# Kernel tuning notes

Measured on AMD Instinct MI355X. Metric: run time of the kernel, lower is better.

Reference implementation:

```python
import jax, jax.numpy as jnp
import numpy as np

B, S, DIM, H = 4, 2048, 1024, 16
DEPTH = DIM // H


def setup_inputs() -> dict:
    key = jax.random.key(0)
    ks = jax.random.split(key, 12)
    s = 0.02
    return {
        "Q": jax.random.normal(ks[0], (B, S, DIM), jnp.float32),
        "K": jax.random.normal(ks[1], (B, S, DIM), jnp.float32),
        "V": jax.random.normal(ks[2], (B, S, DIM), jnp.float32),
        "mask": jax.random.randint(ks[3], (B, 1, 1, S), 0, 2).astype(jnp.float32),
        "Wq": jax.random.normal(ks[4], (DIM, DIM), jnp.float32) * s,
        "bq": jnp.zeros((DIM,), jnp.float32),
        "Wk": jax.random.normal(ks[5], (DIM, DIM), jnp.float32) * s,
        "bk": jnp.zeros((DIM,), jnp.float32),
        "Wv": jax.random.normal(ks[6], (DIM, DIM), jnp.float32) * s,
        "bv": jnp.zeros((DIM,), jnp.float32),
        "Wo": jax.random.normal(ks[7], (DIM, DIM), jnp.float32) * s,
        "bo": jnp.zeros((DIM,), jnp.float32),
    }


def _split_heads(x):
    # [B,S,DIM] -> [B,H,S,DEPTH]
    return x.reshape(x.shape[0], x.shape[1], H, DEPTH).transpose(0, 2, 1, 3)


def reference(Q, K, V, mask, Wq, bq, Wk, bk, Wv, bv, Wo, bo):
    q = _split_heads(Q @ Wq + bq)
    k = _split_heads(K @ Wk + bk)
    v = _split_heads(V @ Wv + bv)
    # scaled dot-product attention; note original scales by sqrt(depth) = last dim of K after split
    logits = jnp.einsum("bhqd,bhkd->bhqk", q, k) / jnp.sqrt(jnp.float32(DEPTH))
    logits = logits + mask * -1e9
    attn = jax.nn.softmax(logits, axis=-1)
    ctx = jnp.einsum("bhqk,bhkd->bhqd", attn, v)
    ctx = ctx.transpose(0, 2, 1, 3).reshape(Q.shape[0], Q.shape[1], DIM)
    return ctx @ Wo + bo
```

## Files before the change

kernel.cpp:

```cpp
#include <hip/hip_runtime.h>

typedef short s16x8 __attribute__((ext_vector_type(8)));
typedef short s16x4 __attribute__((ext_vector_type(4)));
typedef float f32x4 __attribute__((ext_vector_type(4)));

#define MFMA32(a, b, c) __builtin_amdgcn_mfma_f32_16x16x32_bf16((a), (b), (c), 0, 0, 0)

__device__ __forceinline__ void stage16(const unsigned short* g, unsigned short* l) {
#if defined(__HIP_DEVICE_COMPILE__)
  __builtin_amdgcn_global_load_lds((const __attribute__((address_space(1))) unsigned int*)g,
                                   (__attribute__((address_space(3))) unsigned int*)l, 16, 0, 0);
#endif
}

__device__ __forceinline__ unsigned short f2b(float f) {
  unsigned int u = __builtin_bit_cast(unsigned int, f);
  unsigned int r = u + 0x7FFFu + ((u >> 16) & 1u);
  return (unsigned short)(r >> 16);
}
__device__ __forceinline__ unsigned int pk2(float a, float b) {
#if defined(__HIP_DEVICE_COMPILE__)
  unsigned int ua = __builtin_bit_cast(unsigned int, a);
  unsigned int ub = __builtin_bit_cast(unsigned int, b);
  ua += 0x7FFFu + ((ua >> 16) & 1u);
  ub += 0x7FFFu + ((ub >> 16) & 1u);
  return __builtin_amdgcn_perm(ub, ua, 0x07060302u);
#else
  return (unsigned int)f2b(a) | ((unsigned int)f2b(b) << 16);
#endif
}
__device__ __forceinline__ float fast_exp2(float x) {
#if defined(__HIP_DEVICE_COMPILE__) && __has_builtin(__builtin_amdgcn_exp2f)
  return __builtin_amdgcn_exp2f(x);
#else
  return exp2f(x);
#endif
}

__global__ __launch_bounds__(256) void castq(const float* __restrict__ X,
                                             unsigned short* __restrict__ Y) {
  int i = blockIdx.x * 256 + threadIdx.x;
  float4 f0 = ((const float4*)X)[i * 2];
  float4 f1 = ((const float4*)X)[i * 2 + 1];
  uint4 u;
  u.x = pk2(f0.x, f0.y);
  u.y = pk2(f0.z, f0.w);
  u.z = pk2(f1.x, f1.y);
  u.w = pk2(f1.z, f1.w);
  ((uint4*)Y)[i] = u;
}

__global__ void wtrans(const float* __restrict__ W0, const float* __restrict__ W1,
                       const float* __restrict__ W2, const float* __restrict__ W3,
                       unsigned short* __restrict__ T0, unsigned short* __restrict__ T1,
                       unsigned short* __restrict__ T2, unsigned short* __restrict__ T3) {
  const float* W;
  unsigned short* T;
  switch (blockIdx.z) {
    case 0: W = W0; T = T0; break;
    case 1: W = W1; T = T1; break;
    case 2: W = W2; T = T2; break;
    default: W = W3; T = T3; break;
  }
  __shared__ float tile[32][33];
  const int n0 = blockIdx.x << 5;
  const int k0 = blockIdx.y << 5;
  const int tx = threadIdx.x;
  const int ty = threadIdx.y;
#pragma unroll
  for (int j = 0; j < 4; ++j)
    tile[ty + 8 * j][tx] = W[(size_t)(k0 + ty + 8 * j) * 1024 + n0 + tx];
  __syncthreads();
#pragma unroll
  for (int j = 0; j < 4; ++j)
    T[(size_t)(n0 + ty + 8 * j) * 1024 + k0 + tx] = f2b(tile[tx][ty + 8 * j]);
}

template <int MODE>
__global__ __launch_bounds__(256, 3) void gemm_bt(const unsigned short* __restrict__ A,
                                                  const unsigned short* __restrict__ Bt,
                                                  const float* __restrict__ bias,
                                                  void* __restrict__ Cout, float oscale) {
  __shared__ __align__(16) unsigned short As[2 * 128 * 32];
  __shared__ __align__(16) unsigned short Bs[2 * 128 * 32];
  const int n0 = blockIdx.x * 128;
  const int m0 = blockIdx.y * 128;
  const int tid = threadIdx.x;
  const int w = tid >> 6;
  const int lane = tid & 63;
  const int lr = lane & 15;
  const int lg = lane >> 4;
  const int wm = (w >> 1) << 6;
  const int wn = (w & 1) << 6;

  const int srow = w * 16 + (lane >> 2);
  const int sseg = lane & 3;
  const unsigned short* Ag0 = A + (size_t)(m0 + srow) * 1024 + sseg * 8;
  const unsigned short* Ag1 = A + (size_t)(m0 + 64 + srow) * 1024 + sseg * 8;
  const unsigned short* Bg0 = Bt + (size_t)(n0 + srow) * 1024 + sseg * 8;
  const unsigned short* Bg1 = Bt + (size_t)(n0 + 64 + srow) * 1024 + sseg * 8;
  unsigned short* Al0 = &As[(w * 16) * 32];
  unsigned short* Al1 = &As[(64 + w * 16) * 32];
  unsigned short* Bl0 = &Bs[(w * 16) * 32];
  unsigned short* Bl1 = &Bs[(64 + w * 16) * 32];

  f32x4 acc[4][4];
#pragma unroll
  for (int i = 0; i < 4; ++i)
#pragma unroll
    for (int j = 0; j < 4; ++j) {
      f32x4 z = {0.f, 0.f, 0.f, 0.f};
      acc[i][j] = z;
    }

  stage16(Ag0, Al0);
  stage16(Ag1, Al1);
  stage16(Bg0, Bl0);
  stage16(Bg1, Bl1);
  asm volatile("s_waitcnt vmcnt(0)\n\ts_barrier" ::: "memory");

  int cur = 0;
  for (int k0 = 0; k0 < 1024; k0 += 32) {
    if (k0 + 32 < 1024) {
      const int nb = (cur ^ 1) * 4096;
      stage16(Ag0 + k0 + 32, Al0 + nb);
      stage16(Ag1 + k0 + 32, Al1 + nb);
      stage16(Bg0 + k0 + 32, Bl0 + nb);
      stage16(Bg1 + k0 + 32, Bl1 + nb);
    }
    const int cb = cur * 4096;
    s16x8 af[4], bfr[4];
#pragma unroll
    for (int mt = 0; mt < 4; ++mt)
      af[mt] = *(const s16x8*)&As[cb + (wm + mt * 16 + lr) * 32 + lg * 8];
#pragma unroll
    for (int nt = 0; nt < 4; ++nt)
      bfr[nt] = *(const s16x8*)&Bs[cb + (wn + nt * 16 + lr) * 32 + lg * 8];
#pragma unroll
    for (int mt = 0; mt < 4; ++mt)
#pragma unroll
      for (int nt = 0; nt < 4; ++nt)
        acc[mt][nt] = MFMA32(af[mt], bfr[nt], acc[mt][nt]);
    asm volatile("s_waitcnt vmcnt(0)\n\ts_barrier" ::: "memory");
    cur ^= 1;
  }

  float bcol[4];
#pragma unroll
  for (int nt = 0; nt < 4; ++nt) bcol[nt] = bias[n0 + wn + nt * 16 + lr];

#pragma unroll
  for (int mt = 0; mt < 4; ++mt)
#pragma unroll
    for (int nt = 0; nt < 4; ++nt)
#pragma unroll
      for (int r = 0; r < 4; ++r) {
        float v = (acc[mt][nt][r] + bcol[nt]) * oscale;
        int row = m0 + wm + mt * 16 + lg * 4 + r;
        int col = n0 + wn + nt * 16 + lr;
        if constexpr (MODE == 0) {
          int b = row >> 11, s = row & 2047, hh = col >> 6, d = col & 63;
          ((unsigned short*)Cout)[(((size_t)(b * 16 + hh) * 2048 + s) << 6) + d] = f2b(v);
        } else if constexpr (MODE == 1) {
          int b = row >> 11, s = row & 2047, hh = col >> 6, d = col & 63;
          ((unsigned short*)Cout)[(((size_t)(b * 16 + hh) * 64 + d) << 11) + s] = f2b(v);
        } else {
          ((float*)Cout)[(size_t)row * 1024 + col] = v;
        }
      }
}

__global__ __launch_bounds__(256, 4) void flash_attn(const unsigned short* __restrict__ qh,
                                                     const unsigned short* __restrict__ kh,
                                                     const unsigned short* __restrict__ vt,
                                                     const float* __restrict__ mask,
                                                     unsigned short* __restrict__ ctx) {
  const float c2 = 1.4426950408889634e9f;
  const int id = blockIdx.x;
  const int bh = id & 63;
  const int qtile = id >> 6;
  const int b = bh >> 4;
  const int h = bh & 15;
  const int q0 = qtile << 7;
  const int tid = threadIdx.x;
  const int w = tid >> 6;
  const int lane = tid & 63;
  const int lr = lane & 15;
  const int lg = lane >> 4;

  __shared__ __align__(16) unsigned short Ks[2 * 64 * 64];
  __shared__ __align__(16) unsigned short Vs[2 * 64 * 64];

  const unsigned short* qbase = qh + ((size_t)bh * 2048 + q0 + w * 32) * 64;
  const unsigned short* kbase = kh + (size_t)bh * 2048 * 64;
  const unsigned short* vbase = vt + (size_t)bh * 64 * 2048;
  const float* mbase = mask + b * 2048;

  const int rowc = lane >> 3;
  const int gseg = (lane & 7) ^ rowc;
  const unsigned short* kg0 = kbase + (size_t)(w * 16 + rowc) * 64 + gseg * 8;
  const unsigned short* kg1 = kbase + (size_t)(w * 16 + 8 + rowc) * 64 + gseg * 8;
  const unsigned short* vg0 = vbase + (size_t)(w * 16 + rowc) * 2048 + gseg * 8;
  const unsigned short* vg1 = vbase + (size_t)(w * 16 + 8 + rowc) * 2048 + gseg * 8;
  unsigned short* kl0 = &Ks[(w * 16 + 0) * 64];
  unsigned short* kl1 = &Ks[(w * 16 + 8) * 64];
  unsigned short* vl0 = &Vs[(w * 16 + 0) * 64];
  unsigned short* vl1 = &Vs[(w * 16 + 8) * 64];

  s16x8 qf[2][2];
#pragma unroll
  for (int qt = 0; qt < 2; ++qt)
#pragma unroll
    for (int kk = 0; kk < 2; ++kk)
      qf[qt][kk] = *(const s16x8*)(qbase + (qt * 16 + lr) * 64 + kk * 32 + lg * 8);

  const s16x8 ones8 = {(short)0x3F80, (short)0x3F80, (short)0x3F80, (short)0x3F80,
                       (short)0x3F80, (short)0x3F80, (short)0x3F80, (short)0x3F80};

  f32x4 o_acc[2][4];
  f32x4 l_acc[2];
#pragma unroll
  for (int qt = 0; qt < 2; ++qt) {
    f32x4 z = {0.f, 0.f, 0.f, 0.f};
    l_acc[qt] = z;
#pragma unroll
    for (int dt = 0; dt < 4; ++dt) o_acc[qt][dt] = z;
  }

  stage16(kg0, kl0);
  stage16(kg1, kl1);
  stage16(vg0, vl0);
  stage16(vg1, vl1);
  asm volatile("s_waitcnt vmcnt(0)\n\ts_barrier" ::: "memory");

  int cur = 0;
  for (int t0 = 0; t0 < 2048; t0 += 64) {
    if (t0 + 64 < 2048) {
      const int nb = (cur ^ 1) * 4096;
      stage16(kg0 + (size_t)(t0 + 64) * 64, kl0 + nb);
      stage16(kg1 + (size_t)(t0 + 64) * 64, kl1 + nb);
      stage16(vg0 + (t0 + 64), vl0 + nb);
      stage16(vg1 + (t0 + 64), vl1 + nb);
    }
    float4 mk[4];
#pragma unroll
    for (int kt = 0; kt < 4; ++kt) mk[kt] = *(const float4*)(mbase + t0 + kt * 16 + lg * 4);

    const int cb = cur * 4096;
    const int sw = lr & 7;
    unsigned int pw[4][2][2];
#pragma unroll
    for (int kt = 0; kt < 4; ++kt) {
      const int krow = kt * 16 + lr;
      s16x8 kf0 = *(const s16x8*)&Ks[cb + krow * 64 + ((lg ^ sw) * 8)];
      s16x8 kf1 = *(const s16x8*)&Ks[cb + krow * 64 + (((4 + lg) ^ sw) * 8)];
      float ml0 = mk[kt].x * c2, ml1 = mk[kt].y * c2;
      float ml2 = mk[kt].z * c2, ml3 = mk[kt].w * c2;
#pragma unroll
      for (int qt = 0; qt < 2; ++qt) {
        f32x4 s = {0.f, 0.f, 0.f, 0.f};
        s = MFMA32(kf0, qf[qt][0], s);
        s = MFMA32(kf1, qf[qt][1], s);
        pw[kt][qt][0] = pk2(fast_exp2(s[0] - ml0), fast_exp2(s[1] - ml1));
        pw[kt][qt][1] = pk2(fast_exp2(s[2] - ml2), fast_exp2(s[3] - ml3));
      }
    }

#pragma unroll
    for (int c = 0; c < 2; ++c) {
      s16x8 pb[2];
#pragma unroll
      for (int qt = 0; qt < 2; ++qt) {
        uint4 u;
        u.x = pw[2 * c][qt][0];
        u.y = pw[2 * c][qt][1];
        u.z = pw[2 * c + 1][qt][0];
        u.w = pw[2 * c + 1][qt][1];
        pb[qt] = __builtin_bit_cast(s16x8, u);
        l_acc[qt] = MFMA32(ones8, pb[qt], l_acc[qt]);
      }
      const int plo = ((c << 2) | (lg >> 1)) ^ sw;
      const int phi = ((c << 2) | 2 | (lg >> 1)) ^ sw;
      const int sub = (lg & 1) * 4;
#pragma unroll
      for (int dt = 0; dt < 4; ++dt) {
        const int d = dt * 16 + lr;
        s16x4 vlo = *(const s16x4*)&Vs[cb + d * 64 + plo * 8 + sub];
        s16x4 vhi = *(const s16x4*)&Vs[cb + d * 64 + phi * 8 + sub];
        s16x8 vf = __builtin_shufflevector(vlo, vhi, 0, 1, 2, 3, 4, 5, 6, 7);
#pragma unroll
        for (int qt = 0; qt < 2; ++qt) o_acc[qt][dt] = MFMA32(vf, pb[qt], o_acc[qt][dt]);
      }
    }

    asm volatile("s_waitcnt vmcnt(0)\n\ts_barrier" ::: "memory");
    cur ^= 1;
  }

#pragma unroll
  for (int qt = 0; qt < 2; ++qt) {
    float inv = 1.0f / l_acc[qt][0];
    int q = q0 + w * 32 + qt * 16 + lr;
    unsigned short* cp = ctx + ((size_t)(b * 2048 + q) * 16 + h) * 64 + lg * 4;
#pragma unroll
    for (int dt = 0; dt < 4; ++dt) {
      f32x4 o = o_acc[qt][dt];
      uint2 u;
      u.x = pk2(o[0] * inv, o[1] * inv);
      u.y = pk2(o[2] * inv, o[3] * inv);
      *(uint2*)(cp + dt * 16) = u;
    }
  }
}

extern "C" void kernel_launch(void* const* d_in, const int* in_sizes, int n_in,
                              void* d_out, int out_size, void* d_ws, size_t ws_size,
                              hipStream_t stream) {
  (void)in_sizes; (void)n_in; (void)out_size; (void)ws_size;
  const float* Q = (const float*)d_in[0];
  const float* K = (const float*)d_in[1];
  const float* V = (const float*)d_in[2];
  const float* mask = (const float*)d_in[3];
  const float* Wq = (const float*)d_in[4];
  const float* bq = (const float*)d_in[5];
  const float* Wk = (const float*)d_in[6];
  const float* bk = (const float*)d_in[7];
  const float* Wv = (const float*)d_in[8];
  const float* bv = (const float*)d_in[9];
  const float* Wo = (const float*)d_in[10];
  const float* bo = (const float*)d_in[11];

  char* ws = (char*)d_ws;
  unsigned short* wqt = (unsigned short*)(ws + (size_t)0);
  unsigned short* wkt = (unsigned short*)(ws + ((size_t)2 << 20));
  unsigned short* wvt = (unsigned short*)(ws + ((size_t)4 << 20));
  unsigned short* wot = (unsigned short*)(ws + ((size_t)6 << 20));
  unsigned short* qhb = (unsigned short*)(ws + ((size_t)8 << 20));
  unsigned short* khb = (unsigned short*)(ws + ((size_t)24 << 20));
  unsigned short* vtb = (unsigned short*)(ws + ((size_t)40 << 20));
  unsigned short* tmp = (unsigned short*)(ws + ((size_t)56 << 20));
  unsigned short* ctx = tmp;

  wtrans<<<dim3(32, 32, 4), dim3(32, 8), 0, stream>>>(Wq, Wk, Wv, Wo, wqt, wkt, wvt, wot);

  const float qscale = 0.18033688011112042f;
  dim3 gg(8, 64), bb(256);
  const int castBlocks = (8192 * 1024) / (256 * 8);

  castq<<<castBlocks, 256, 0, stream>>>(Q, tmp);
  gemm_bt<0><<<gg, bb, 0, stream>>>(tmp, wqt, bq, qhb, qscale);
  castq<<<castBlocks, 256, 0, stream>>>(K, tmp);
  gemm_bt<0><<<gg, bb, 0, stream>>>(tmp, wkt, bk, khb, 1.0f);
  castq<<<castBlocks, 256, 0, stream>>>(V, tmp);
  gemm_bt<1><<<gg, bb, 0, stream>>>(tmp, wvt, bv, vtb, 1.0f);

  flash_attn<<<dim3(1024), dim3(256), 0, stream>>>(qhb, khb, vtb, mask, ctx);

  gemm_bt<2><<<gg, bb, 0, stream>>>(ctx, wot, bo, d_out, 1.0f);
}
```

Measured before the change: 389.3 us.

## Fuse fp32-to-bf16 cast into QKV GEMM and batch three projections in one launch

Removes the three separate castq kernels and their bf16 scratch round-trips. The new QKV GEMM loads fp32 activations directly, packs them to bf16 in registers and writes them to LDS, while B is still staged asynchronously. The three projections run as one grid with z=3 instead of three sequential launches. In exchange, each A tile reads twice the global bytes, and the conversion work sits inside the GEMM main loop, which may add latency.

```diff
diff --git a/kernel.cpp b/kernel.cpp
--- a/kernel.cpp
+++ b/kernel.cpp
@@ -35,19 +35,6 @@
 #else
   return exp2f(x);
 #endif
-}
-
-__global__ __launch_bounds__(256) void castq(const float* __restrict__ X,
-                                             unsigned short* __restrict__ Y) {
-  int i = blockIdx.x * 256 + threadIdx.x;
-  float4 f0 = ((const float4*)X)[i * 2];
-  float4 f1 = ((const float4*)X)[i * 2 + 1];
-  uint4 u;
-  u.x = pk2(f0.x, f0.y);
-  u.y = pk2(f0.z, f0.w);
-  u.z = pk2(f1.x, f1.y);
-  u.w = pk2(f1.z, f1.w);
-  ((uint4*)Y)[i] = u;
 }
 
 __global__ void wtrans(const float* __restrict__ W0, const float* __restrict__ W1,
@@ -76,11 +63,24 @@
     T[(size_t)(n0 + ty + 8 * j) * 1024 + k0 + tx] = f2b(tile[tx][ty + 8 * j]);
 }
 
-template <int MODE>
-__global__ __launch_bounds__(256, 3) void gemm_bt(const unsigned short* __restrict__ A,
-                                                  const unsigned short* __restrict__ Bt,
-                                                  const float* __restrict__ bias,
-                                                  void* __restrict__ Cout, float oscale) {
+__global__ __launch_bounds__(256, 3) void gemm_qkv(
+    const float* __restrict__ Qf, const float* __restrict__ Kf, const float* __restrict__ Vf,
+    const unsigned short* __restrict__ Wqt, const unsigned short* __restrict__ Wkt,
+    const unsigned short* __restrict__ Wvt, const float* __restrict__ bq,
+    const float* __restrict__ bk, const float* __restrict__ bv,
+    unsigned short* __restrict__ qh, unsigned short* __restrict__ kh,
+    unsigned short* __restrict__ vtb, float qscale) {
+  const float* A;
+  const unsigned short* Bt;
+  const float* bias;
+  unsigned short* Cout;
+  float oscale = 1.0f;
+  int vmode = 0;
+  switch (blockIdx.z) {
+    case 0: A = Qf; Bt = Wqt; bias = bq; Cout = qh; oscale = qscale; break;
+    case 1: A = Kf; Bt = Wkt; bias = bk; Cout = kh; break;
+    default: A = Vf; Bt = Wvt; bias = bv; Cout = vtb; vmode = 1; break;
+  }
   __shared__ __align__(16) unsigned short As[2 * 128 * 32];
   __shared__ __align__(16) unsigned short Bs[2 * 128 * 32];
   const int n0 = blockIdx.x * 128;
@@ -95,6 +95,132 @@
 
   const int srow = w * 16 + (lane >> 2);
   const int sseg = lane & 3;
+  const float* Ag0 = A + (size_t)(m0 + srow) * 1024 + sseg * 8;
+  const float* Ag1 = A + (size_t)(m0 + 64 + srow) * 1024 + sseg * 8;
+  const unsigned short* Bg0 = Bt + (size_t)(n0 + srow) * 1024 + sseg * 8;
+  const unsigned short* Bg1 = Bt + (size_t)(n0 + 64 + srow) * 1024 + sseg * 8;
+  unsigned short* Bl0 = &Bs[(w * 16) * 32];
+  unsigned short* Bl1 = &Bs[(64 + w * 16) * 32];
+  const int aoff0 = (w * 16) * 32 + lane * 8;
+  const int aoff1 = (64 + w * 16) * 32 + lane * 8;
+
+  f32x4 acc[4][4];
+#pragma unroll
+  for (int i = 0; i < 4; ++i)
+#pragma unroll
+    for (int j = 0; j < 4; ++j) {
+      f32x4 z = {0.f, 0.f, 0.f, 0.f};
+      acc[i][j] = z;
+    }
+
+  {
+    float4 a0lo = *(const float4*)Ag0;
+    float4 a0hi = *(const float4*)(Ag0 + 4);
+    float4 a1lo = *(const float4*)Ag1;
+    float4 a1hi = *(const float4*)(Ag1 + 4);
+    stage16(Bg0, Bl0);
+    stage16(Bg1, Bl1);
+    uint4 u0, u1;
+    u0.x = pk2(a0lo.x, a0lo.y); u0.y = pk2(a0lo.z, a0lo.w);
+    u0.z = pk2(a0hi.x, a0hi.y); u0.w = pk2(a0hi.z, a0hi.w);
+    u1.x = pk2(a1lo.x, a1lo.y); u1.y = pk2(a1lo.z, a1lo.w);
+    u1.z = pk2(a1hi.x, a1hi.y); u1.w = pk2(a1hi.z, a1hi.w);
+    *(uint4*)&As[aoff0] = u0;
+    *(uint4*)&As[aoff1] = u1;
+  }
+  asm volatile("s_waitcnt vmcnt(0) lgkmcnt(0)\n\ts_barrier" ::: "memory");
+
+  int cur = 0;
+  for (int k0 = 0; k0 < 1024; k0 += 32) {
+    const bool next = (k0 + 32) < 1024;
+    float4 a0lo, a0hi, a1lo, a1hi;
+    if (next) {
+      a0lo = *(const float4*)(Ag0 + k0 + 32);
+      a0hi = *(const float4*)(Ag0 + k0 + 36);
+      a1lo = *(const float4*)(Ag1 + k0 + 32);
+      a1hi = *(const float4*)(Ag1 + k0 + 36);
+      const int nb = (cur ^ 1) * 4096;
+      stage16(Bg0 + k0 + 32, Bl0 + nb);
+      stage16(Bg1 + k0 + 32, Bl1 + nb);
+    }
+    const int cb = cur * 4096;
+    s16x8 af[4], bfr[4];
+#pragma unroll
+    for (int mt = 0; mt < 4; ++mt)
+      af[mt] = *(const s16x8*)&As[cb + (wm + mt * 16 + lr) * 32 + lg * 8];
+#pragma unroll
+    for (int nt = 0; nt < 4; ++nt)
+      bfr[nt] = *(const s16x8*)&Bs[cb + (wn + nt * 16 + lr) * 32 + lg * 8];
+#pragma unroll
+    for (int mt = 0; mt < 4; ++mt)
+#pragma unroll
+      for (int nt = 0; nt < 4; ++nt)
+        acc[mt][nt] = MFMA32(af[mt], bfr[nt], acc[mt][nt]);
+    if (next) {
+      const int nb = (cur ^ 1) * 4096;
+      uint4 u0, u1;
+      u0.x = pk2(a0lo.x, a0lo.y); u0.y = pk2(a0lo.z, a0lo.w);
+      u0.z = pk2(a0hi.x, a0hi.y); u0.w = pk2(a0hi.z, a0hi.w);
+      u1.x = pk2(a1lo.x, a1lo.y); u1.y = pk2(a1lo.z, a1lo.w);
+      u1.z = pk2(a1hi.x, a1hi.y); u1.w = pk2(a1hi.z, a1hi.w);
+      *(uint4*)&As[nb + aoff0] = u0;
+      *(uint4*)&As[nb + aoff1] = u1;
+    }
+    asm volatile("s_waitcnt vmcnt(0) lgkmcnt(0)\n\ts_barrier" ::: "memory");
+    cur ^= 1;
+  }
+
+  float bcol[4];
+#pragma unroll
+  for (int nt = 0; nt < 4; ++nt) bcol[nt] = bias[n0 + wn + nt * 16 + lr];
+
+  if (vmode == 0) {
+#pragma unroll
+    for (int mt = 0; mt < 4; ++mt)
+#pragma unroll
+      for (int nt = 0; nt < 4; ++nt)
+#pragma unroll
+        for (int r = 0; r < 4; ++r) {
+          float v = (acc[mt][nt][r] + bcol[nt]) * oscale;
+          int row = m0 + wm + mt * 16 + lg * 4 + r;
+          int col = n0 + wn + nt * 16 + lr;
+          int b = row >> 11, s = row & 2047, hh = col >> 6, d = col & 63;
+          Cout[(((size_t)(b * 16 + hh) * 2048 + s) << 6) + d] = f2b(v);
+        }
+  } else {
+#pragma unroll
+    for (int mt = 0; mt < 4; ++mt)
+#pragma unroll
+      for (int nt = 0; nt < 4; ++nt)
+#pragma unroll
+        for (int r = 0; r < 4; ++r) {
+          float v = acc[mt][nt][r] + bcol[nt];
+          int row = m0 + wm + mt * 16 + lg * 4 + r;
+          int col = n0 + wn + nt * 16 + lr;
+          int b = row >> 11, s = row & 2047, hh = col >> 6, d = col & 63;
+          Cout[(((size_t)(b * 16 + hh) * 64 + d) << 11) + s] = f2b(v);
+        }
+  }
+}
+
+__global__ __launch_bounds__(256, 3) void gemm_out(const unsigned short* __restrict__ A,
+                                                   const unsigned short* __restrict__ Bt,
+                                                   const float* __restrict__ bias,
+                                                   float* __restrict__ Cout) {
+  __shared__ __align__(16) unsigned short As[2 * 128 * 32];
+  __shared__ __align__(16) unsigned short Bs[2 * 128 * 32];
+  const int n0 = blockIdx.x * 128;
+  const int m0 = blockIdx.y * 128;
+  const int tid = threadIdx.x;
+  const int w = tid >> 6;
+  const int lane = tid & 63;
+  const int lr = lane & 15;
+  const int lg = lane >> 4;
+  const int wm = (w >> 1) << 6;
+  const int wn = (w & 1) << 6;
+
+  const int srow = w * 16 + (lane >> 2);
+  const int sseg = lane & 3;
   const unsigned short* Ag0 = A + (size_t)(m0 + srow) * 1024 + sseg * 8;
   const unsigned short* Ag1 = A + (size_t)(m0 + 64 + srow) * 1024 + sseg * 8;
   const unsigned short* Bg0 = Bt + (size_t)(n0 + srow) * 1024 + sseg * 8;
@@ -155,18 +281,10 @@
     for (int nt = 0; nt < 4; ++nt)
 #pragma unroll
       for (int r = 0; r < 4; ++r) {
-        float v = (acc[mt][nt][r] + bcol[nt]) * oscale;
+        float v = acc[mt][nt][r] + bcol[nt];
         int row = m0 + wm + mt * 16 + lg * 4 + r;
         int col = n0 + wn + nt * 16 + lr;
-        if constexpr (MODE == 0) {
-          int b = row >> 11, s = row & 2047, hh = col >> 6, d = col & 63;
-          ((unsigned short*)Cout)[(((size_t)(b * 16 + hh) * 2048 + s) << 6) + d] = f2b(v);
-        } else if constexpr (MODE == 1) {
-          int b = row >> 11, s = row & 2047, hh = col >> 6, d = col & 63;
-          ((unsigned short*)Cout)[(((size_t)(b * 16 + hh) * 64 + d) << 11) + s] = f2b(v);
-        } else {
-          ((float*)Cout)[(size_t)row * 1024 + col] = v;
-        }
+        Cout[(size_t)row * 1024 + col] = v;
       }
 }
 
@@ -338,23 +456,16 @@
   unsigned short* qhb = (unsigned short*)(ws + ((size_t)8 << 20));
   unsigned short* khb = (unsigned short*)(ws + ((size_t)24 << 20));
   unsigned short* vtb = (unsigned short*)(ws + ((size_t)40 << 20));
-  unsigned short* tmp = (unsigned short*)(ws + ((size_t)56 << 20));
-  unsigned short* ctx = tmp;
+  unsigned short* ctx = (unsigned short*)(ws + ((size_t)56 << 20));
 
   wtrans<<<dim3(32, 32, 4), dim3(32, 8), 0, stream>>>(Wq, Wk, Wv, Wo, wqt, wkt, wvt, wot);
 
   const float qscale = 0.18033688011112042f;
-  dim3 gg(8, 64), bb(256);
-  const int castBlocks = (8192 * 1024) / (256 * 8);
-
-  castq<<<castBlocks, 256, 0, stream>>>(Q, tmp);
-  gemm_bt<0><<<gg, bb, 0, stream>>>(tmp, wqt, bq, qhb, qscale);
-  castq<<<castBlocks, 256, 0, stream>>>(K, tmp);
-  gemm_bt<0><<<gg, bb, 0, stream>>>(tmp, wkt, bk, khb, 1.0f);
-  castq<<<castBlocks, 256, 0, stream>>>(V, tmp);
-  gemm_bt<1><<<gg, bb, 0, stream>>>(tmp, wvt, bv, vtb, 1.0f);
+
+  gemm_qkv<<<dim3(8, 64, 3), dim3(256), 0, stream>>>(Q, K, V, wqt, wkt, wvt, bq, bk, bv,
+                                                     qhb, khb, vtb, qscale);
 
   flash_attn<<<dim3(1024), dim3(256), 0, stream>>>(qhb, khb, vtb, mask, ctx);
 
-  gemm_bt<2><<<gg, bb, 0, stream>>>(ctx, wot, bo, d_out, 1.0f);
-}
+  gemm_out<<<dim3(8, 64), dim3(256), 0, stream>>>(ctx, wot, bo, (float*)d_out);
+}
```

After: 379.8 us. -2.4%, faster.
